# Kernel tuning notes

Hardware: AMD Instinct MI355X
Metric: run time of the kernel (lower is better)

Reference implementation:

```python
import jax, jax.numpy as jnp
import numpy as np

K = 3          # per-row / per-col topk, from init kwarg k
THRESHOLD = 0.0


def setup_inputs() -> dict:
    key = jax.random.key(0)
    k1, k2 = jax.random.split(key)
    P, R, S = 512, 256, 256
    matching_score_map = jax.random.normal(k1, (P, R, S), dtype=jnp.float32)
    node_corr_scores = jax.random.uniform(k2, (P,), dtype=jnp.float32)
    ref_knn_masks = jnp.ones((P, R), dtype=bool)
    src_knn_masks = jnp.ones((P, S), dtype=bool)
    return {
        "matching_score_map": matching_score_map,
        "node_corr_scores": node_corr_scores,
        "ref_knn_masks": ref_knn_masks,
        "src_knn_masks": src_knn_masks,
    }


def reference(matching_score_map, node_corr_scores, ref_knn_masks, src_knn_masks):
    # score map: exp of log-matching scores  [P, R, S]
    score = jnp.exp(matching_score_map)
    P, R, S = score.shape
    # valid correspondence mask  [P, R, S]
    corr_mask = ref_knn_masks[:, :, None] & src_knn_masks[:, None, :]

    p_idx = jnp.arange(P)[:, None, None]

    # topk along src axis (dim=2), scatter back into a zero map
    ref_vals, ref_idx = jax.lax.top_k(score, K)                      # [P, R, K]
    ref_score_map = jnp.zeros_like(score).at[
        p_idx, jnp.arange(R)[None, :, None], ref_idx
    ].set(ref_vals)

    # topk along ref axis (dim=1): transpose so it is the last axis
    src_vals, src_idx = jax.lax.top_k(score.transpose(0, 2, 1), K)   # [P, S, K]
    src_score_map = jnp.zeros_like(score).at[
        p_idx, src_idx, jnp.arange(S)[None, :, None]
    ].set(src_vals)

    ref_corr_map = (ref_score_map > THRESHOLD) & corr_mask
    src_corr_map = (src_score_map > THRESHOLD) & corr_mask

    score_map = (ref_score_map + src_score_map) * 0.5
    # mutual=False -> logical_or; conditional=False -> no node_corr_scores scaling
    corr_map = ref_corr_map | src_corr_map
    return score_map, corr_map
```

## Files before the change

### kernel.cpp

```cpp
#include <hip/hip_runtime.h>
#include <math.h>
#include <stdint.h>

#define Pn 512
#define Rn 256
#define Sn 256

typedef unsigned long long u64;
typedef unsigned int u32;

__device__ __forceinline__ u32 mono(float f) {
  u32 u = __float_as_uint(f);
  return (u & 0x80000000u) ? ~u : (u | 0x80000000u);
}
__device__ __forceinline__ float unmono(u32 m) {
  u32 bits = (m & 0x80000000u) ? (m & 0x7FFFFFFFu) : ~m;
  return __uint_as_float(bits);
}
__device__ __forceinline__ u64 makekey(float v, int idx) {
  return ((u64)mono(v) << 32) | (u32)(~(u32)idx);
}
__device__ __forceinline__ int key_idx(u64 k) { return (int)(~(u32)k); }
__device__ __forceinline__ float key_val(u64 k) { return unmono((u32)(k >> 32)); }
__device__ __forceinline__ void cswap(u64& a, u64& b) {
  const bool c = a > b;
  const u64 hi = c ? a : b;
  const u64 lo = c ? b : a;
  a = hi; b = lo;
}

__device__ __forceinline__ void ins3f(float v, int i,
    float& t0, int& i0, float& t1, int& i1, float& t2, int& i2) {
  const bool b0 = v > t0, b1 = v > t1, b2 = v > t2;
  const float nt0 = b0 ? v : t0;
  const int   ni0 = b0 ? i : i0;
  const float nt1 = b0 ? t0 : (b1 ? v : t1);
  const int   ni1 = b0 ? i0 : (b1 ? i : i1);
  const float nt2 = b1 ? t1 : (b2 ? v : t2);
  const int   ni2 = b1 ? i1 : (b2 ? i : i2);
  t0 = nt0; i0 = ni0; t1 = nt1; i1 = ni1; t2 = nt2; i2 = ni2;
}

#define COLSLAB_BLOCKS (Pn * 4)
#define ROW_BLOCKS ((Pn * Rn) / 4)

__global__ __launch_bounds__(256) void top3_kernel(
    const float* __restrict__ score,
    float* __restrict__ refv, int* __restrict__ refi,
    float* __restrict__ colpv, int* __restrict__ colpi) {
  const size_t PS = (size_t)Pn * Sn;
  if (blockIdx.x < COLSLAB_BLOCKS) {
    const int p    = blockIdx.x >> 2;
    const int slab = blockIdx.x & 3;
    const int s    = threadIdx.x;
    const float* base = score + (size_t)p * Rn * Sn + (size_t)slab * 64 * Sn + s;
    float t0 = -INFINITY, t1 = -INFINITY, t2 = -INFINITY;
    int   i0 = -1, i1 = -1, i2 = -1;
    const int r0 = slab * 64;
    #pragma unroll 8
    for (int r = 0; r < 64; ++r)
      ins3f(base[(size_t)r * Sn], r0 + r, t0, i0, t1, i1, t2, i2);
    const size_t o = (size_t)p * Sn + s;
    colpv[(slab * 3 + 0) * PS + o] = t0; colpi[(slab * 3 + 0) * PS + o] = i0;
    colpv[(slab * 3 + 1) * PS + o] = t1; colpi[(slab * 3 + 1) * PS + o] = i1;
    colpv[(slab * 3 + 2) * PS + o] = t2; colpi[(slab * 3 + 2) * PS + o] = i2;
  } else {
    const int bid  = blockIdx.x - COLSLAB_BLOCKS;
    const int row  = (bid * blockDim.x + threadIdx.x) >> 6;
    const int lane = threadIdx.x & 63;
    const float4 v = reinterpret_cast<const float4*>(score + (size_t)row * Sn)[lane];
    const int b = lane * 4;
    u64 a0 = makekey(v.x, b + 0);
    u64 a1 = makekey(v.y, b + 1);
    u64 a2 = makekey(v.z, b + 2);
    u64 a3 = makekey(v.w, b + 3);
    cswap(a0, a1); cswap(a2, a3); cswap(a0, a2); cswap(a1, a3); cswap(a1, a2);
    u64 t0 = a0, t1 = a1, t2 = a2;

    u64 res0 = 0, res1 = 0, res2 = 0;
    #pragma unroll
    for (int j = 0; j < 3; ++j) {
      u64 m = t0;
      #pragma unroll
      for (int off = 1; off < 64; off <<= 1) {
        const u64 o = __shfl_xor(m, off);
        m = (o > m) ? o : m;
      }
      const bool hit = (t0 == m);
      t0 = hit ? t1 : t0;
      t1 = hit ? t2 : t1;
      t2 = hit ? 0ull : t2;
      if (j == 0) res0 = m; else if (j == 1) res1 = m; else res2 = m;
    }
    if (lane == 0) {
      const size_t o = (size_t)row * 3;
      refv[o + 0] = expf(key_val(res0)); refi[o + 0] = key_idx(res0);
      refv[o + 1] = expf(key_val(res1)); refi[o + 1] = key_idx(res1);
      refv[o + 2] = expf(key_val(res2)); refi[o + 2] = key_idx(res2);
    }
  }
}

__device__ __forceinline__ void compute_elem(
    int s, int r, bool rmask, int sm,
    float rv0, float rv1, float rv2, int ri0, int ri1, int ri2,
    float a0, int b0, float a1, int b1, float a2, int b2,
    float& oscore, float& ocorr) {
  const float rv = (s == ri0) ? rv0 : (s == ri1) ? rv1 : (s == ri2) ? rv2 : 0.0f;
  const float sv = (r == b0) ? a0 : (r == b1) ? a1 : (r == b2) ? a2 : 0.0f;
  oscore = 0.5f * (rv + sv);
  const bool m = rmask && (sm != 0);
  ocorr = (((rv > 0.0f) || (sv > 0.0f)) && m) ? 1.0f : 0.0f;
}

__global__ __launch_bounds__(256) void write_kernel(
    const float* __restrict__ refv, const int* __restrict__ refi,
    const float* __restrict__ colpv, const int* __restrict__ colpi,
    const int* __restrict__ rmaskp, const int* __restrict__ smaskp,
    float* __restrict__ out) {
  const int p     = blockIdx.x >> 2;
  const int rbase = (blockIdx.x & 3) * 64;
  const int warp  = threadIdx.x >> 6;
  const int lane  = threadIdx.x & 63;
  const size_t PS = (size_t)Pn * Sn;
  const size_t N  = (size_t)Pn * Rn * Sn;
  const size_t cb = (size_t)p * Sn;

  float4 T0 = reinterpret_cast<const float4*>(colpv + 0 * PS + cb)[lane];
  float4 T1 = reinterpret_cast<const float4*>(colpv + 1 * PS + cb)[lane];
  float4 T2 = reinterpret_cast<const float4*>(colpv + 2 * PS + cb)[lane];
  int4   I0 = reinterpret_cast<const int4*>(colpi + 0 * PS + cb)[lane];
  int4   I1 = reinterpret_cast<const int4*>(colpi + 1 * PS + cb)[lane];
  int4   I2 = reinterpret_cast<const int4*>(colpi + 2 * PS + cb)[lane];
  #pragma unroll
  for (int sk = 3; sk < 12; ++sk) {
    const float4 V = reinterpret_cast<const float4*>(colpv + (size_t)sk * PS + cb)[lane];
    const int4   I = reinterpret_cast<const int4*>(colpi + (size_t)sk * PS + cb)[lane];
    ins3f(V.x, I.x, T0.x, I0.x, T1.x, I1.x, T2.x, I2.x);
    ins3f(V.y, I.y, T0.y, I0.y, T1.y, I1.y, T2.y, I2.y);
    ins3f(V.z, I.z, T0.z, I0.z, T1.z, I1.z, T2.z, I2.z);
    ins3f(V.w, I.w, T0.w, I0.w, T1.w, I1.w, T2.w, I2.w);
  }
  T0.x = expf(T0.x); T0.y = expf(T0.y); T0.z = expf(T0.z); T0.w = expf(T0.w);
  T1.x = expf(T1.x); T1.y = expf(T1.y); T1.z = expf(T1.z); T1.w = expf(T1.w);
  T2.x = expf(T2.x); T2.y = expf(T2.y); T2.z = expf(T2.z); T2.w = expf(T2.w);

  const int4 sm = reinterpret_cast<const int4*>(smaskp + cb)[lane];
  const int sbase = lane * 4;
  float* outp = out + (size_t)p * Rn * Sn;

  #pragma unroll 4
  for (int it = 0; it < 16; ++it) {
    const int r   = rbase + it * 4 + warp;
    const int row = p * Rn + r;
    const size_t rb = (size_t)row * 3;
    const float rv0 = refv[rb + 0], rv1 = refv[rb + 1], rv2 = refv[rb + 2];
    const int   ri0 = refi[rb + 0], ri1 = refi[rb + 1], ri2 = refi[rb + 2];
    const bool  rm  = rmaskp[row] != 0;

    float4 osc, oco;
    compute_elem(sbase + 0, r, rm, sm.x, rv0, rv1, rv2, ri0, ri1, ri2,
                 T0.x, I0.x, T1.x, I1.x, T2.x, I2.x, osc.x, oco.x);
    compute_elem(sbase + 1, r, rm, sm.y, rv0, rv1, rv2, ri0, ri1, ri2,
                 T0.y, I0.y, T1.y, I1.y, T2.y, I2.y, osc.y, oco.y);
    compute_elem(sbase + 2, r, rm, sm.z, rv0, rv1, rv2, ri0, ri1, ri2,
                 T0.z, I0.z, T1.z, I1.z, T2.z, I2.z, osc.z, oco.z);
    compute_elem(sbase + 3, r, rm, sm.w, rv0, rv1, rv2, ri0, ri1, ri2,
                 T0.w, I0.w, T1.w, I1.w, T2.w, I2.w, osc.w, oco.w);

    reinterpret_cast<float4*>(outp + (size_t)r * Sn)[lane]     = osc;
    reinterpret_cast<float4*>(outp + N + (size_t)r * Sn)[lane] = oco;
  }
}

extern "C" void kernel_launch(void* const* d_in, const int* in_sizes, int n_in,
                              void* d_out, int out_size, void* d_ws, size_t ws_size,
                              hipStream_t stream) {
  const float* score = (const float*)d_in[0];
  const int* rmask = (const int*)d_in[2];
  const int* smask = (const int*)d_in[3];
  float* out = (float*)d_out;

  const size_t PR = (size_t)Pn * Rn;
  const size_t PS = (size_t)Pn * Sn;
  float* refv  = (float*)d_ws;
  int*   refi  = (int*)(refv + 3 * PR);
  float* colpv = (float*)(refi + 3 * PR);
  int*   colpi = (int*)(colpv + 12 * PS);

  top3_kernel<<<COLSLAB_BLOCKS + ROW_BLOCKS, 256, 0, stream>>>(
      score, refv, refi, colpv, colpi);
  write_kernel<<<(Pn * Rn) / 64, 256, 0, stream>>>(
      refv, refi, colpv, colpi, rmask, smask, out);
}
```

Before: 466.2 us.

## Fuse per-row top-3 selection into the output write kernel

```diff
diff --git a/kernel.cpp b/kernel.cpp
--- a/kernel.cpp
+++ b/kernel.cpp
@@ -41,64 +41,24 @@
   t0 = nt0; i0 = ni0; t1 = nt1; i1 = ni1; t2 = nt2; i2 = ni2;
 }
 
-#define COLSLAB_BLOCKS (Pn * 4)
-#define ROW_BLOCKS ((Pn * Rn) / 4)
-
-__global__ __launch_bounds__(256) void top3_kernel(
+__global__ __launch_bounds__(256) void colslab_kernel(
     const float* __restrict__ score,
-    float* __restrict__ refv, int* __restrict__ refi,
     float* __restrict__ colpv, int* __restrict__ colpi) {
   const size_t PS = (size_t)Pn * Sn;
-  if (blockIdx.x < COLSLAB_BLOCKS) {
-    const int p    = blockIdx.x >> 2;
-    const int slab = blockIdx.x & 3;
-    const int s    = threadIdx.x;
-    const float* base = score + (size_t)p * Rn * Sn + (size_t)slab * 64 * Sn + s;
-    float t0 = -INFINITY, t1 = -INFINITY, t2 = -INFINITY;
-    int   i0 = -1, i1 = -1, i2 = -1;
-    const int r0 = slab * 64;
-    #pragma unroll 8
-    for (int r = 0; r < 64; ++r)
-      ins3f(base[(size_t)r * Sn], r0 + r, t0, i0, t1, i1, t2, i2);
-    const size_t o = (size_t)p * Sn + s;
-    colpv[(slab * 3 + 0) * PS + o] = t0; colpi[(slab * 3 + 0) * PS + o] = i0;
-    colpv[(slab * 3 + 1) * PS + o] = t1; colpi[(slab * 3 + 1) * PS + o] = i1;
-    colpv[(slab * 3 + 2) * PS + o] = t2; colpi[(slab * 3 + 2) * PS + o] = i2;
-  } else {
-    const int bid  = blockIdx.x - COLSLAB_BLOCKS;
-    const int row  = (bid * blockDim.x + threadIdx.x) >> 6;
-    const int lane = threadIdx.x & 63;
-    const float4 v = reinterpret_cast<const float4*>(score + (size_t)row * Sn)[lane];
-    const int b = lane * 4;
-    u64 a0 = makekey(v.x, b + 0);
-    u64 a1 = makekey(v.y, b + 1);
-    u64 a2 = makekey(v.z, b + 2);
-    u64 a3 = makekey(v.w, b + 3);
-    cswap(a0, a1); cswap(a2, a3); cswap(a0, a2); cswap(a1, a3); cswap(a1, a2);
-    u64 t0 = a0, t1 = a1, t2 = a2;
-
-    u64 res0 = 0, res1 = 0, res2 = 0;
-    #pragma unroll
-    for (int j = 0; j < 3; ++j) {
-      u64 m = t0;
-      #pragma unroll
-      for (int off = 1; off < 64; off <<= 1) {
-        const u64 o = __shfl_xor(m, off);
-        m = (o > m) ? o : m;
-      }
-      const bool hit = (t0 == m);
-      t0 = hit ? t1 : t0;
-      t1 = hit ? t2 : t1;
-      t2 = hit ? 0ull : t2;
-      if (j == 0) res0 = m; else if (j == 1) res1 = m; else res2 = m;
-    }
-    if (lane == 0) {
-      const size_t o = (size_t)row * 3;
-      refv[o + 0] = expf(key_val(res0)); refi[o + 0] = key_idx(res0);
-      refv[o + 1] = expf(key_val(res1)); refi[o + 1] = key_idx(res1);
-      refv[o + 2] = expf(key_val(res2)); refi[o + 2] = key_idx(res2);
-    }
-  }
+  const int p    = blockIdx.x >> 2;
+  const int slab = blockIdx.x & 3;
+  const int s    = threadIdx.x;
+  const float* base = score + (size_t)p * Rn * Sn + (size_t)slab * 64 * Sn + s;
+  float t0 = -INFINITY, t1 = -INFINITY, t2 = -INFINITY;
+  int   i0 = -1, i1 = -1, i2 = -1;
+  const int r0 = slab * 64;
+  #pragma unroll 8
+  for (int r = 0; r < 64; ++r)
+    ins3f(base[(size_t)r * Sn], r0 + r, t0, i0, t1, i1, t2, i2);
+  const size_t o = (size_t)p * Sn + s;
+  colpv[(slab * 3 + 0) * PS + o] = t0; colpi[(slab * 3 + 0) * PS + o] = i0;
+  colpv[(slab * 3 + 1) * PS + o] = t1; colpi[(slab * 3 + 1) * PS + o] = i1;
+  colpv[(slab * 3 + 2) * PS + o] = t2; colpi[(slab * 3 + 2) * PS + o] = i2;
 }
 
 __device__ __forceinline__ void compute_elem(
@@ -114,7 +74,7 @@
 }
 
 __global__ __launch_bounds__(256) void write_kernel(
-    const float* __restrict__ refv, const int* __restrict__ refi,
+    const float* __restrict__ score,
     const float* __restrict__ colpv, const int* __restrict__ colpi,
     const int* __restrict__ rmaskp, const int* __restrict__ smaskp,
     float* __restrict__ out) {
@@ -147,16 +107,40 @@
 
   const int4 sm = reinterpret_cast<const int4*>(smaskp + cb)[lane];
   const int sbase = lane * 4;
+  const float* tile = score + (size_t)p * Rn * Sn;
   float* outp = out + (size_t)p * Rn * Sn;
 
-  #pragma unroll 4
+  #pragma unroll 2
   for (int it = 0; it < 16; ++it) {
-    const int r   = rbase + it * 4 + warp;
-    const int row = p * Rn + r;
-    const size_t rb = (size_t)row * 3;
-    const float rv0 = refv[rb + 0], rv1 = refv[rb + 1], rv2 = refv[rb + 2];
-    const int   ri0 = refi[rb + 0], ri1 = refi[rb + 1], ri2 = refi[rb + 2];
-    const bool  rm  = rmaskp[row] != 0;
+    const int r = rbase + it * 4 + warp;
+    const float4 v = reinterpret_cast<const float4*>(tile + (size_t)r * Sn)[lane];
+    const int b = lane * 4;
+    u64 a0 = makekey(v.x, b + 0);
+    u64 a1 = makekey(v.y, b + 1);
+    u64 a2 = makekey(v.z, b + 2);
+    u64 a3 = makekey(v.w, b + 3);
+    cswap(a0, a1); cswap(a2, a3); cswap(a0, a2); cswap(a1, a3); cswap(a1, a2);
+    u64 t0 = a0, t1 = a1, t2 = a2;
+    u64 res0 = 0, res1 = 0, res2 = 0;
+    #pragma unroll
+    for (int j = 0; j < 3; ++j) {
+      u64 m = t0;
+      #pragma unroll
+      for (int off = 1; off < 64; off <<= 1) {
+        const u64 o = __shfl_xor(m, off);
+        m = (o > m) ? o : m;
+      }
+      const bool hit = (t0 == m);
+      t0 = hit ? t1 : t0;
+      t1 = hit ? t2 : t1;
+      t2 = hit ? 0ull : t2;
+      if (j == 0) res0 = m; else if (j == 1) res1 = m; else res2 = m;
+    }
+    const float rv0 = expf(key_val(res0));
+    const float rv1 = expf(key_val(res1));
+    const float rv2 = expf(key_val(res2));
+    const int   ri0 = key_idx(res0), ri1 = key_idx(res1), ri2 = key_idx(res2);
+    const bool  rm  = rmaskp[p * Rn + r] != 0;
 
     float4 osc, oco;
     compute_elem(sbase + 0, r, rm, sm.x, rv0, rv1, rv2, ri0, ri1, ri2,
@@ -181,15 +165,11 @@
   const int* smask = (const int*)d_in[3];
   float* out = (float*)d_out;
 
-  const size_t PR = (size_t)Pn * Rn;
   const size_t PS = (size_t)Pn * Sn;
-  float* refv  = (float*)d_ws;
-  int*   refi  = (int*)(refv + 3 * PR);
-  float* colpv = (float*)(refi + 3 * PR);
+  float* colpv = (float*)d_ws;
   int*   colpi = (int*)(colpv + 12 * PS);
 
-  top3_kernel<<<COLSLAB_BLOCKS + ROW_BLOCKS, 256, 0, stream>>>(
-      score, refv, refi, colpv, colpi);
-  write_kernel<<<(Pn * Rn) / 64, 256, 0, stream>>>(
-      refv, refi, colpv, colpi, rmask, smask, out);
+  colslab_kernel<<<Pn * 4, 256, 0, stream>>>(score, colpv, colpi);
+  write_kernel<<<Pn * 4, 256, 0, stream>>>(score, colpv, colpi,
+                                           rmask, smask, out);
 }
```

Measured after the change: 420.9 us. 1.11x faster.
